# Performance work log

Hardware: AMD Instinct MI355X
Metric: run time of the kernel (lower is better)

## Reference

```python
import jax, jax.numpy as jnp
import numpy as np

N = 50000        # n_nodes
E = 640000       # n_edges
D = 128          # d_model (in_dim == out_dim)
H = 8            # num_heads
DH = D // H      # head dim = 16
EPS = 1e-5


def _batchnorm(x, g, b):
    # BatchNorm1d, training-mode batch statistics (biased variance)
    mu = jnp.mean(x, axis=0)
    var = jnp.mean((x - mu) ** 2, axis=0)
    return (x - mu) * jax.lax.rsqrt(var + EPS) * g + b


def setup_inputs() -> dict:
    key = jax.random.key(0)
    ks = jax.random.split(key, 16)
    s = 0.05
    h = jax.random.normal(ks[0], (N, D), jnp.float32)
    src = jax.random.randint(ks[1], (E,), 0, N)
    # guarantee every node has >= 1 incoming edge (avoids z == 0)
    dst = jnp.concatenate([jnp.arange(N), jax.random.randint(ks[2], (E - N,), 0, N)])
    return {
        "h": h,
        "src": src,
        "dst": dst,
        "WQ": jax.random.normal(ks[3], (D, D), jnp.float32) * s,
        "WK": jax.random.normal(ks[4], (D, D), jnp.float32) * s,
        "WV": jax.random.normal(ks[5], (D, D), jnp.float32) * s,
        "WO": jax.random.normal(ks[6], (D, D), jnp.float32) * s,
        "bO": jnp.zeros((D,), jnp.float32),
        "W1": jax.random.normal(ks[7], (2 * D, D), jnp.float32) * s,
        "b1": jnp.zeros((2 * D,), jnp.float32),
        "W2": jax.random.normal(ks[8], (D, 2 * D), jnp.float32) * s,
        "b2": jnp.zeros((D,), jnp.float32),
        "bn1_g": jnp.ones((D,), jnp.float32),
        "bn1_b": jnp.zeros((D,), jnp.float32),
        "bn2_g": jnp.ones((D,), jnp.float32),
        "bn2_b": jnp.zeros((D,), jnp.float32),
    }


def reference(h, src, dst, WQ, WK, WV, WO, bO, W1, b1, W2, b2, bn1_g, bn1_b, bn2_g, bn2_b):
    n = h.shape[0]
    # projections -> [N, H, DH]
    Q = (h @ WQ.T).reshape(n, H, DH)
    K = (h @ WK.T).reshape(n, H, DH)
    V = (h @ WV.T).reshape(n, H, DH)
    # per-edge score: sum(K[src] * Q[dst]) -> [E, H]; clamp/exp (scaled_exp)
    score = jnp.sum(K[src] * Q[dst], axis=-1) / np.sqrt(DH)
    score = jnp.exp(jnp.clip(score, -5.0, 5.0))
    # scatter-sum weighted values and normalizers to destination nodes
    wV = jax.ops.segment_sum(V[src] * score[..., None], dst, num_segments=n)  # [N,H,DH]
    z = jax.ops.segment_sum(score, dst, num_segments=n)                       # [N,H]
    attn = (wV / z[..., None]).reshape(n, D)
    # O projection + residual + BN1
    h1 = _batchnorm(h + (attn @ WO.T + bO), bn1_g, bn1_b)
    # FFN + residual + BN2
    f = jax.nn.relu(h1 @ W1.T + b1) @ W2.T + b2
    return _batchnorm(h1 + f, bn2_g, bn2_b)
```

## Files before the change

kernel.cpp:

```cpp
#include <hip/hip_runtime.h>
#include <math.h>


#define ND128 16384
typedef _Float16 f16;
typedef __attribute__((ext_vector_type(8))) _Float16 h8;
typedef __attribute__((ext_vector_type(4))) _Float16 h4;
typedef __attribute__((ext_vector_type(2))) _Float16 h2;
typedef __attribute__((ext_vector_type(4))) float f4;
typedef __attribute__((ext_vector_type(2))) float ff2;

__device__ __forceinline__ float fast_exp2(float x) {
#if __has_builtin(__builtin_amdgcn_exp2f)
    return __builtin_amdgcn_exp2f(x);
#else
    return exp2f(x);
#endif
}

template <int CTRL>
__device__ __forceinline__ float dppadd(float x) {
    int t = __builtin_amdgcn_update_dpp(0, __float_as_int(x), CTRL, 0xF, 0xF, false);
    return x + __int_as_float(t);
}
__device__ __forceinline__ float wsum8(float p) {
    p = dppadd<0xB1>(p);
    p = dppadd<0x4E>(p);
    p = dppadd<0x141>(p);
    return p;
}

__device__ __forceinline__ ff2 fp8x2_dec(unsigned v) {
#if __has_builtin(__builtin_amdgcn_cvt_pk_f32_fp8)
    return __builtin_amdgcn_cvt_pk_f32_fp8((int)v, false);
#else
    ff2 r;
    unsigned b0 = v & 0xffu, b1 = (v >> 8) & 0xffu;
    {
        unsigned e = (b0 >> 3) & 15u, m = b0 & 7u;
        float x = e ? __uint_as_float(((e + 120u) << 23) | (m << 20)) : (float)m * 0.001953125f;
        r.x = (b0 & 0x80u) ? -x : x;
    }
    {
        unsigned e = (b1 >> 3) & 15u, m = b1 & 7u;
        float x = e ? __uint_as_float(((e + 120u) << 23) | (m << 20)) : (float)m * 0.001953125f;
        r.y = (b1 & 0x80u) ? -x : x;
    }
    return r;
#endif
}

#if !__has_builtin(__builtin_amdgcn_cvt_pk_fp8_f32)
__device__ __forceinline__ unsigned char fp8_1(float f) {
    float a = fabsf(f);
    unsigned sg = (__float_as_uint(f) >> 31) << 7;
    if (a >= 448.f) return (unsigned char)(sg | 0x7E);
    if (a < 0.0009765625f) return (unsigned char)sg;
    int E; float m = frexpf(a, &E);
    if (E - 1 < -6) {
        int q = (int)rintf(a * 512.f);
        if (q > 7) return (unsigned char)(sg | 0x08);
        return (unsigned char)(sg | q);
    }
    int q = (int)rintf(m * 16.f);
    if (q == 16) { q = 8; E += 1; }
    int Ef = E - 1 + 7;
    if (Ef > 15) return (unsigned char)(sg | 0x7E);
    return (unsigned char)(sg | (Ef << 3) | (q - 8));
}
#endif

__device__ __forceinline__ unsigned fp8_pack4(float a0, float a1, float a2, float a3) {
#if __has_builtin(__builtin_amdgcn_cvt_pk_fp8_f32)
    int pk = __builtin_amdgcn_cvt_pk_fp8_f32(a0, a1, 0, false);
    pk = __builtin_amdgcn_cvt_pk_fp8_f32(a2, a3, pk, true);
    return (unsigned)pk;
#else
    return (unsigned)fp8_1(a0) | ((unsigned)fp8_1(a1) << 8) |
           ((unsigned)fp8_1(a2) << 16) | ((unsigned)fp8_1(a3) << 24);
#endif
}

__global__ __launch_bounds__(256) void k_prep_hist(
    const float* __restrict__ h, f16* __restrict__ hb,
    const float* __restrict__ WQ, const float* __restrict__ WK,
    const float* __restrict__ WV, const float* __restrict__ WO,
    const float* __restrict__ W2,
    f16* __restrict__ Wqb, f16* __restrict__ Wkb,
    f16* __restrict__ Wvb, f16* __restrict__ Wob, f16* __restrict__ W2b,
    int* __restrict__ cursor, const int* __restrict__ dst,
    int N, int E, int nhb)
{
    const int tid = threadIdx.x;
    if (blockIdx.x < (unsigned)nhb) {
        int e = blockIdx.x * 256 + tid;
        if (e < E) atomicAdd(&cursor[dst[e]], 1);
        return;
    }
    const int p = blockIdx.x - nhb;
    const int slab = p >> 1, my = p & 1;
#pragma unroll
    for (int it2 = 0; it2 < 4; ++it2) {
        int it = my * 4 + it2;
        int cid = it * 256 + tid;
        int lane = cid & 63;
        int m = (cid >> 6) & 7;
        int kb = cid >> 9;
        int row = slab * 128 + m * 16 + (lane & 15);
        int col = kb * 32 + (lane >> 4) * 8;
        f16 o8[8];
        if (row < N) {
            const float* pp = h + (size_t)row * 128 + col;
            float4 f0 = *(const float4*)pp;
            float4 f1 = *(const float4*)(pp + 4);
            o8[0] = (f16)f0.x; o8[1] = (f16)f0.y; o8[2] = (f16)f0.z; o8[3] = (f16)f0.w;
            o8[4] = (f16)f1.x; o8[5] = (f16)f1.y; o8[6] = (f16)f1.z; o8[7] = (f16)f1.w;
        } else {
#pragma unroll
            for (int j = 0; j < 8; ++j) o8[j] = (f16)0.f;
        }
        *(h8*)(hb + (size_t)slab * ND128 + (size_t)cid * 8) = *(const h8*)o8;
    }
    if (slab < 6 && my == 1) {
        const float* Wsrc; f16* dstw; int K, base;
        if (slab < 4) {
            Wsrc = slab == 0 ? WQ : slab == 1 ? WK : slab == 2 ? WV : WO;
            dstw = slab == 0 ? Wqb : slab == 1 ? Wkb : slab == 2 ? Wvb : Wob;
            K = 128; base = 0;
        } else {
            Wsrc = W2; dstw = W2b; K = 256; base = (slab - 4) * 2048;
        }
#pragma unroll
        for (int it = 0; it < 8; ++it) {
            int cid = base + it * 256 + tid;
            int lane = cid & 63;
            int kb, nt;
            if (K == 128) { kb = (cid >> 6) & 3; nt = cid >> 8; }
            else          { kb = (cid >> 6) & 7; nt = cid >> 9; }
            int row = nt * 16 + (lane & 15);
            int col = kb * 32 + (lane >> 4) * 8;
            const float* pp = Wsrc + (size_t)row * K + col;
            f16 o8[8];
#pragma unroll
            for (int j = 0; j < 8; ++j) o8[j] = (f16)pp[j];
            *(h8*)(dstw + (size_t)cid * 8) = *(const h8*)o8;
        }
    }
}

__global__ __launch_bounds__(256) void k_qkv(
    const f16* __restrict__ hb, const f16* __restrict__ Wqb,
    const f16* __restrict__ Wkb, const f16* __restrict__ Wvb,
    f16* __restrict__ Qb, unsigned char* __restrict__ KV8, int N)
{
    const int slab = blockIdx.x, oidx = blockIdx.y, mh = blockIdx.z;
    const int w = threadIdx.x >> 6, lane = threadIdx.x & 63;
    const f16* __restrict__ Wb = oidx == 0 ? Wqb : oidx == 1 ? Wkb : Wvb;
    const f16* A = hb + (size_t)slab * ND128;

    h8 bfr[2][4];
#pragma unroll
    for (int nt = 0; nt < 2; ++nt)
#pragma unroll
        for (int kb = 0; kb < 4; ++kb)
            bfr[nt][kb] = *(const h8*)(Wb + (size_t)(((2 * w + nt) * 4 + kb) * 64 + lane) * 8);

    f4 acc[4][2];
    f4 zero = {0.f, 0.f, 0.f, 0.f};
#pragma unroll
    for (int m = 0; m < 4; ++m) { acc[m][0] = zero; acc[m][1] = zero; }

#pragma unroll
    for (int m = 0; m < 4; ++m) {
        int mg = mh * 4 + m;
#pragma unroll
        for (int kb = 0; kb < 4; ++kb) {
            h8 a = *(const h8*)(A + (size_t)((kb * 8 + mg) * 64 + lane) * 8);
            acc[m][0] = __builtin_amdgcn_mfma_f32_16x16x32_f16(bfr[0][kb], a, acc[m][0], 0, 0, 0);
            acc[m][1] = __builtin_amdgcn_mfma_f32_16x16x32_f16(bfr[1][kb], a, acc[m][1], 0, 0, 0);
        }
    }

    const int rl = lane & 15, quad = lane >> 4;
    if (oidx == 0) {
#pragma unroll
        for (int m = 0; m < 4; ++m) {
            int gr = slab * 128 + (mh * 4 + m) * 16 + rl;
            if (gr < N) {
#pragma unroll
                for (int nt = 0; nt < 2; ++nt) {
                    h4 o;
                    o[0] = (f16)acc[m][nt][0]; o[1] = (f16)acc[m][nt][1];
                    o[2] = (f16)acc[m][nt][2]; o[3] = (f16)acc[m][nt][3];
                    *(h4*)(Qb + (size_t)gr * 128 + w * 32 + nt * 16 + quad * 4) = o;
                }
            }
        }
    } else {
        const int voff = (oidx == 2) ? 128 : 0;
#pragma unroll
        for (int m = 0; m < 4; ++m) {
            int gr = slab * 128 + (mh * 4 + m) * 16 + rl;
            if (gr < N) {
#pragma unroll
                for (int nt = 0; nt < 2; ++nt) {
                    unsigned pk = fp8_pack4(acc[m][nt][0], acc[m][nt][1],
                                            acc[m][nt][2], acc[m][nt][3]);
                    *(unsigned*)(KV8 + (size_t)gr * 256 + voff + w * 32 + nt * 16 + quad * 4) = pk;
                }
            }
        }
    }
}

__global__ __launch_bounds__(256) void k_scanA(
    const int* __restrict__ cnt, int* __restrict__ bsum, int N)
{
    const int t = threadIdx.x;
    int base = blockIdx.x * 2048 + t * 8;
    int s = 0;
#pragma unroll
    for (int j = 0; j < 8; ++j) {
        int idx = base + j;
        if (idx < N) s += cnt[idx];
    }
#pragma unroll
    for (int off = 32; off; off >>= 1) s += __shfl_down(s, off, 64);
    __shared__ int ws4[4];
    if ((t & 63) == 0) ws4[t >> 6] = s;
    __syncthreads();
    if (t == 0) bsum[blockIdx.x] = ws4[0] + ws4[1] + ws4[2] + ws4[3];
}

__global__ __launch_bounds__(256) void k_scanC(
    const int* __restrict__ cnt, const int* __restrict__ bsum,
    int* __restrict__ rowptr, int* __restrict__ cursor, int N, int nsb)
{
    const int t = threadIdx.x, b = blockIdx.x;
    __shared__ int sboff;
    if (t == 0) {
        int r = 0;
        for (int i2 = 0; i2 < b; ++i2) r += bsum[i2];
        sboff = r;
    }
    if (t == 64 && b == nsb - 1) {
        int r = 0;
        for (int i2 = 0; i2 < nsb; ++i2) r += bsum[i2];
        rowptr[N] = r;
    }
    int base = b * 2048 + t * 8;
    int loc[8];
    int s = 0;
#pragma unroll
    for (int j = 0; j < 8; ++j) {
        int idx = base + j;
        loc[j] = (idx < N) ? cnt[idx] : 0;
        s += loc[j];
    }
    __shared__ int part[256];
    part[t] = s;
    __syncthreads();
    for (int off = 1; off < 256; off <<= 1) {
        int v = (t >= off) ? part[t - off] : 0;
        __syncthreads();
        part[t] += v;
        __syncthreads();
    }
    int run = sboff + (t ? part[t - 1] : 0);
#pragma unroll
    for (int j = 0; j < 8; ++j) {
        int idx = base + j;
        if (idx < N) { rowptr[idx] = run; cursor[idx] = run; run += loc[j]; }
    }
}

__global__ __launch_bounds__(256) void k_scatter(
    const int* __restrict__ src, const int* __restrict__ dst,
    int* __restrict__ cursor, int* __restrict__ csr_src, int E)
{
    int e = blockIdx.x * 256 + threadIdx.x;
    if (e < E) {
        int pos = atomicAdd(&cursor[dst[e]], 1);
        csr_src[pos] = src[e];
    }
}

__global__ __launch_bounds__(256) void k_attn(
    const f16* __restrict__ Qb, const unsigned char* __restrict__ KV8,
    const int* __restrict__ rowptr, const int* __restrict__ csr_src,
    f16* __restrict__ attnf, int N)
{
    const int node = blockIdx.x * 4 + (threadIdx.x >> 6);
    const int lane = threadIdx.x & 63;
    if (node >= N) return;
    const int beg = rowptr[node], end = rowptr[node + 1];

    float qx, qy;
    {
        h2 q2 = ((const h2*)(Qb + (size_t)node * 128))[lane];
        const float SCL = 0.25f * 1.44269504f;
        qx = (float)q2[0] * SCL;
        qy = (float)q2[1] * SCL;
    }
    const float CLP = 5.f * 1.44269504f;

    float axA = 0.f, ayA = 0.f, axB = 0.f, ayB = 0.f, zA = 0.f, zB = 0.f;
    int i = beg;
    for (; i + 3 < end; i += 4) {
        int s0 = csr_src[i], s1 = csr_src[i + 1];
        int s2 = csr_src[i + 2], s3 = csr_src[i + 3];
        unsigned k0 = *(const unsigned short*)(KV8 + (size_t)s0 * 256 + 2 * lane);
        unsigned k1 = *(const unsigned short*)(KV8 + (size_t)s1 * 256 + 2 * lane);
        unsigned k2 = *(const unsigned short*)(KV8 + (size_t)s2 * 256 + 2 * lane);
        unsigned k3 = *(const unsigned short*)(KV8 + (size_t)s3 * 256 + 2 * lane);
        unsigned v0 = *(const unsigned short*)(KV8 + (size_t)s0 * 256 + 128 + 2 * lane);
        unsigned v1 = *(const unsigned short*)(KV8 + (size_t)s1 * 256 + 128 + 2 * lane);
        unsigned v2 = *(const unsigned short*)(KV8 + (size_t)s2 * 256 + 128 + 2 * lane);
        unsigned v3 = *(const unsigned short*)(KV8 + (size_t)s3 * 256 + 128 + 2 * lane);
        ff2 kf0 = fp8x2_dec(k0), kf1 = fp8x2_dec(k1);
        ff2 kf2 = fp8x2_dec(k2), kf3 = fp8x2_dec(k3);
        float p0 = fmaf(qx, kf0.x, qy * kf0.y);
        float p1 = fmaf(qx, kf1.x, qy * kf1.y);
        float p2 = fmaf(qx, kf2.x, qy * kf2.y);
        float p3 = fmaf(qx, kf3.x, qy * kf3.y);
        p0 = wsum8(p0); p1 = wsum8(p1); p2 = wsum8(p2); p3 = wsum8(p3);
        float sc0 = fast_exp2(fminf(fmaxf(p0, -CLP), CLP));
        float sc1 = fast_exp2(fminf(fmaxf(p1, -CLP), CLP));
        float sc2 = fast_exp2(fminf(fmaxf(p2, -CLP), CLP));
        float sc3 = fast_exp2(fminf(fmaxf(p3, -CLP), CLP));
        ff2 vf0 = fp8x2_dec(v0), vf1 = fp8x2_dec(v1);
        ff2 vf2 = fp8x2_dec(v2), vf3 = fp8x2_dec(v3);
        axA = fmaf(vf0.x, sc0, axA); ayA = fmaf(vf0.y, sc0, ayA);
        axB = fmaf(vf1.x, sc1, axB); ayB = fmaf(vf1.y, sc1, ayB);
        axA = fmaf(vf2.x, sc2, axA); ayA = fmaf(vf2.y, sc2, ayA);
        axB = fmaf(vf3.x, sc3, axB); ayB = fmaf(vf3.y, sc3, ayB);
        zA += sc0 + sc2; zB += sc1 + sc3;
    }
    for (; i < end; ++i) {
        int s0 = csr_src[i];
        unsigned k0 = *(const unsigned short*)(KV8 + (size_t)s0 * 256 + 2 * lane);
        unsigned v0 = *(const unsigned short*)(KV8 + (size_t)s0 * 256 + 128 + 2 * lane);
        ff2 kf0 = fp8x2_dec(k0);
        float p0 = fmaf(qx, kf0.x, qy * kf0.y);
        p0 = wsum8(p0);
        float sc0 = fast_exp2(fminf(fmaxf(p0, -CLP), CLP));
        ff2 vf0 = fp8x2_dec(v0);
        axA = fmaf(vf0.x, sc0, axA); ayA = fmaf(vf0.y, sc0, ayA);
        zA += sc0;
    }
    float inv = 1.f / (zA + zB);
    h2 o2;
    o2[0] = (f16)((axA + axB) * inv);
    o2[1] = (f16)((ayA + ayB) * inv);
    int slab = node >> 7, m = (node >> 4) & 7, lr = node & 15;
    int kb = lane >> 4, quad2 = (lane & 15) >> 2, j = (lane & 3) * 2;
    *(h2*)(attnf + (size_t)slab * ND128 +
           (size_t)(((kb * 8 + m) * 64 + lr + 16 * quad2) * 8 + j)) = o2;
}

__global__ __launch_bounds__(256) void k_oproj(
    const f16* __restrict__ attnf, const f16* __restrict__ Wob,
    const f16* __restrict__ hbf, const float* __restrict__ bO,
    f16* __restrict__ t1b, float* __restrict__ bn, int N)
{
    __shared__ float csum[128], csq[128];
    const int tid = threadIdx.x, slab = blockIdx.x, mh = blockIdx.y;
    const int w = tid >> 6, lane = tid & 63;
    if (tid < 128) { csum[tid] = 0.f; csq[tid] = 0.f; }
    __syncthreads();
    const f16* A = attnf + (size_t)slab * ND128;
    const f16* HB = hbf + (size_t)slab * ND128;

    h8 bfr[2][4];
#pragma unroll
    for (int nt = 0; nt < 2; ++nt)
#pragma unroll
        for (int kb = 0; kb < 4; ++kb)
            bfr[nt][kb] = *(const h8*)(Wob + (size_t)(((2 * w + nt) * 4 + kb) * 64 + lane) * 8);

    f4 acc[2][2];
    f4 zero = {0.f, 0.f, 0.f, 0.f};
#pragma unroll
    for (int m = 0; m < 2; ++m) { acc[m][0] = zero; acc[m][1] = zero; }
#pragma unroll
    for (int m = 0; m < 2; ++m) {
        int mg = mh * 2 + m;
#pragma unroll
        for (int kb = 0; kb < 4; ++kb) {
            h8 a = *(const h8*)(A + (size_t)((kb * 8 + mg) * 64 + lane) * 8);
            acc[m][0] = __builtin_amdgcn_mfma_f32_16x16x32_f16(bfr[0][kb], a, acc[m][0], 0, 0, 0);
            acc[m][1] = __builtin_amdgcn_mfma_f32_16x16x32_f16(bfr[1][kb], a, acc[m][1], 0, 0, 0);
        }
    }

    const int rl = lane & 15, quad = lane >> 4;
    float4 bo[2];
#pragma unroll
    for (int nt = 0; nt < 2; ++nt)
        bo[nt] = *(const float4*)(bO + w * 32 + nt * 16 + quad * 4);
    float pcs[2][4], pcq[2][4];
#pragma unroll
    for (int nt = 0; nt < 2; ++nt)
#pragma unroll
        for (int r = 0; r < 4; ++r) { pcs[nt][r] = 0.f; pcq[nt][r] = 0.f; }

#pragma unroll
    for (int m = 0; m < 2; ++m) {
        int mg = mh * 2 + m;
        int gr = slab * 128 + mg * 16 + rl;
        if (gr < N) {
#pragma unroll
            for (int nt = 0; nt < 2; ++nt) {
                size_t fidx = (size_t)(((w * 8 + mg) * 64 + (nt * 2 + (quad >> 1)) * 16 + rl) * 8 +
                                       (quad & 1) * 4);
                h4 hv4 = *(const h4*)(HB + fidx);
                float v0 = acc[m][nt][0] + (float)hv4[0] + bo[nt].x;
                float v1 = acc[m][nt][1] + (float)hv4[1] + bo[nt].y;
                float v2 = acc[m][nt][2] + (float)hv4[2] + bo[nt].z;
                float v3 = acc[m][nt][3] + (float)hv4[3] + bo[nt].w;
                h4 o; o[0] = (f16)v0; o[1] = (f16)v1; o[2] = (f16)v2; o[3] = (f16)v3;
                *(h4*)(t1b + (size_t)slab * ND128 + fidx) = o;
                pcs[nt][0] += v0; pcq[nt][0] += v0 * v0;
                pcs[nt][1] += v1; pcq[nt][1] += v1 * v1;
                pcs[nt][2] += v2; pcq[nt][2] += v2 * v2;
                pcs[nt][3] += v3; pcq[nt][3] += v3 * v3;
            }
        }
    }
#pragma unroll
    for (int nt = 0; nt < 2; ++nt)
#pragma unroll
        for (int r = 0; r < 4; ++r) {
            float s = pcs[nt][r], q = pcq[nt][r];
            s += __shfl_xor(s, 8, 16); q += __shfl_xor(q, 8, 16);
            s += __shfl_xor(s, 4, 16); q += __shfl_xor(q, 4, 16);
            s += __shfl_xor(s, 2, 16); q += __shfl_xor(q, 2, 16);
            s += __shfl_xor(s, 1, 16); q += __shfl_xor(q, 1, 16);
            if (rl == 0) {
                int cl = w * 32 + nt * 16 + quad * 4 + r;
                atomicAdd(&csum[cl], s);
                atomicAdd(&csq[cl], q);
            }
        }
    __syncthreads();
    if (tid < 128) {
        atomicAdd(bn + tid, csum[tid]);
        atomicAdd(bn + 128 + tid, csq[tid]);
    }
}

__global__ __launch_bounds__(128) void k_fold1(
    const float* __restrict__ bn, const float* __restrict__ g1,
    const float* __restrict__ bb1, const float* __restrict__ W1,
    const float* __restrict__ b1, f16* __restrict__ W1b,
    float* __restrict__ badj, float* __restrict__ sfold,
    float* __restrict__ bfold, int N)
{
    const int o = blockIdx.x, i = threadIdx.x;
    float invN = 1.f / (float)N;
    float mu = bn[i] * invN;
    float var = bn[128 + i] * invN - mu * mu;
    float s = g1[i] * rsqrtf(var + 1e-5f);
    float bb = bb1[i] - mu * s;
    if (o == 0) { sfold[i] = s; bfold[i] = bb; }
    float wv = W1[(size_t)o * 128 + i];
    __shared__ float red[128];
    red[i] = wv * bb;
    const int nt = o >> 4, lanelow = o & 15;
    const int kb = i >> 5, quad = (i >> 3) & 3, j = i & 7;
    W1b[(size_t)(((nt * 4 + kb) * 64 + lanelow + 16 * quad) * 8 + j)] = (f16)(wv * s);
    __syncthreads();
#pragma unroll
    for (int off = 64; off; off >>= 1) {
        if (i < off) red[i] += red[i + off];
        __syncthreads();
    }
    if (i == 0) badj[o] = b1[o] + red[0];
}

__global__ __launch_bounds__(256) void k_ffn1(
    const f16* __restrict__ t1b, const f16* __restrict__ W1b,
    const float* __restrict__ badj, f16* __restrict__ ub, int N)
{
    const int slab = blockIdx.x, ch = blockIdx.y, mh = blockIdx.z;
    const int w = threadIdx.x >> 6, lane = threadIdx.x & 63;
    const f16* A = t1b + (size_t)slab * ND128;

    h8 bfr[2][4];
#pragma unroll
    for (int nt = 0; nt < 2; ++nt)
#pragma unroll
        for (int kb = 0; kb < 4; ++kb) {
            int ntg = ch * 8 + 2 * w + nt;
            bfr[nt][kb] = *(const h8*)(W1b + (size_t)((ntg * 4 + kb) * 64 + lane) * 8);
        }

    f4 acc[4][2];
    f4 zero = {0.f, 0.f, 0.f, 0.f};
#pragma unroll
    for (int m = 0; m < 4; ++m) { acc[m][0] = zero; acc[m][1] = zero; }
#pragma unroll
    for (int m = 0; m < 4; ++m) {
        int mg = mh * 4 + m;
#pragma unroll
        for (int kb = 0; kb < 4; ++kb) {
            h8 a = *(const h8*)(A + (size_t)((kb * 8 + mg) * 64 + lane) * 8);
            acc[m][0] = __builtin_amdgcn_mfma_f32_16x16x32_f16(bfr[0][kb], a, acc[m][0], 0, 0, 0);
            acc[m][1] = __builtin_amdgcn_mfma_f32_16x16x32_f16(bfr[1][kb], a, acc[m][1], 0, 0, 0);
        }
    }

    const int rl = lane & 15, quad = lane >> 4;
    const int kbu = ch * 4 + w;
    float4 ba[2];
#pragma unroll
    for (int nt = 0; nt < 2; ++nt)
        ba[nt] = *(const float4*)(badj + ch * 128 + w * 32 + nt * 16 + quad * 4);
#pragma unroll
    for (int m = 0; m < 4; ++m) {
        int mg = mh * 4 + m;
        int gr = slab * 128 + mg * 16 + rl;
        if (gr < N) {
#pragma unroll
            for (int nt = 0; nt < 2; ++nt) {
                h4 o;
                o[0] = (f16)fmaxf(acc[m][nt][0] + ba[nt].x, 0.f);
                o[1] = (f16)fmaxf(acc[m][nt][1] + ba[nt].y, 0.f);
                o[2] = (f16)fmaxf(acc[m][nt][2] + ba[nt].z, 0.f);
                o[3] = (f16)fmaxf(acc[m][nt][3] + ba[nt].w, 0.f);
                *(h4*)(ub + (size_t)slab * 32768 +
                       (size_t)(((kbu * 8 + mg) * 64 + (nt * 2 + (quad >> 1)) * 16 + rl) * 8 +
                                (quad & 1) * 4)) = o;
            }
        }
    }
}

__global__ __launch_bounds__(256) void k_ffn2(
    const f16* __restrict__ ub, const f16* __restrict__ W2b,
    const f16* __restrict__ t1b,
    const float* __restrict__ sfold, const float* __restrict__ bfold,
    const float* __restrict__ b2, float* __restrict__ out,
    float* __restrict__ bn, int N)
{
    __shared__ float csum[128], csq[128], sS[128], sB[128];
    const int tid = threadIdx.x, slab = blockIdx.x, mh = blockIdx.y;
    const int w = tid >> 6, lane = tid & 63;
    if (tid < 128) {
        csum[tid] = 0.f; csq[tid] = 0.f;
        sS[tid] = sfold[tid]; sB[tid] = bfold[tid] + b2[tid];
    }
    __syncthreads();
    const f16* A = ub + (size_t)slab * 32768;
    const f16* T1 = t1b + (size_t)slab * ND128;

    h8 bfr[2][8];
#pragma unroll
    for (int nt = 0; nt < 2; ++nt)
#pragma unroll
        for (int kb = 0; kb < 8; ++kb)
            bfr[nt][kb] = *(const h8*)(W2b + (size_t)(((2 * w + nt) * 8 + kb) * 64 + lane) * 8);

    f4 acc[2][2];
    f4 zero = {0.f, 0.f, 0.f, 0.f};
#pragma unroll
    for (int m = 0; m < 2; ++m) { acc[m][0] = zero; acc[m][1] = zero; }
#pragma unroll
    for (int m = 0; m < 2; ++m) {
        int mg = mh * 2 + m;
#pragma unroll
        for (int kb = 0; kb < 8; ++kb) {
            h8 a = *(const h8*)(A + (size_t)((kb * 8 + mg) * 64 + lane) * 8);
            acc[m][0] = __builtin_amdgcn_mfma_f32_16x16x32_f16(bfr[0][kb], a, acc[m][0], 0, 0, 0);
            acc[m][1] = __builtin_amdgcn_mfma_f32_16x16x32_f16(bfr[1][kb], a, acc[m][1], 0, 0, 0);
        }
    }

    const int rl = lane & 15, quad = lane >> 4;
    float pcs[2][4], pcq[2][4];
#pragma unroll
    for (int nt = 0; nt < 2; ++nt)
#pragma unroll
        for (int r = 0; r < 4; ++r) { pcs[nt][r] = 0.f; pcq[nt][r] = 0.f; }

#pragma unroll
    for (int m = 0; m < 2; ++m) {
        int mg = mh * 2 + m;
        int gr = slab * 128 + mg * 16 + rl;
        if (gr < N) {
#pragma unroll
            for (int nt = 0; nt < 2; ++nt) {
                int col0 = w * 32 + nt * 16 + quad * 4;
                h4 t1v = *(const h4*)(T1 +
                    (size_t)(((w * 8 + mg) * 64 + (nt * 2 + (quad >> 1)) * 16 + rl) * 8 +
                             (quad & 1) * 4));
                float4 ss = *(const float4*)&sS[col0];
                float4 sb = *(const float4*)&sB[col0];
                float4 o;
                o.x = acc[m][nt][0] + fmaf(ss.x, (float)t1v[0], sb.x);
                o.y = acc[m][nt][1] + fmaf(ss.y, (float)t1v[1], sb.y);
                o.z = acc[m][nt][2] + fmaf(ss.z, (float)t1v[2], sb.z);
                o.w = acc[m][nt][3] + fmaf(ss.w, (float)t1v[3], sb.w);
                *(float4*)(out + (size_t)gr * 128 + col0) = o;
                pcs[nt][0] += o.x; pcq[nt][0] += o.x * o.x;
                pcs[nt][1] += o.y; pcq[nt][1] += o.y * o.y;
                pcs[nt][2] += o.z; pcq[nt][2] += o.z * o.z;
                pcs[nt][3] += o.w; pcq[nt][3] += o.w * o.w;
            }
        }
    }
#pragma unroll
    for (int nt = 0; nt < 2; ++nt)
#pragma unroll
        for (int r = 0; r < 4; ++r) {
            float s = pcs[nt][r], q = pcq[nt][r];
            s += __shfl_xor(s, 8, 16); q += __shfl_xor(q, 8, 16);
            s += __shfl_xor(s, 4, 16); q += __shfl_xor(q, 4, 16);
            s += __shfl_xor(s, 2, 16); q += __shfl_xor(q, 2, 16);
            s += __shfl_xor(s, 1, 16); q += __shfl_xor(q, 1, 16);
            if (rl == 0) {
                int cl = w * 32 + nt * 16 + quad * 4 + r;
                atomicAdd(&csum[cl], s);
                atomicAdd(&csq[cl], q);
            }
        }
    __syncthreads();
    if (tid < 128) {
        atomicAdd(bn + 256 + tid, csum[tid]);
        atomicAdd(bn + 384 + tid, csq[tid]);
    }
}

__global__ __launch_bounds__(256) void k_bn2(
    float* __restrict__ out, const float* __restrict__ bn,
    const float* __restrict__ g2, const float* __restrict__ bb2, int N)
{
    __shared__ float sS[128], sB[128];
    const int tid = threadIdx.x;
    if (tid < 128) {
        float invN = 1.f / (float)N;
        float mu = bn[256 + tid] * invN;
        float var = bn[384 + tid] * invN - mu * mu;
        float scl = g2[tid] * rsqrtf(var + 1e-5f);
        sS[tid] = scl;
        sB[tid] = bb2[tid] - mu * scl;
    }
    __syncthreads();
    size_t idx = (size_t)blockIdx.x * 256 + tid;
    size_t total = (size_t)N * 32;
    if (idx < total) {
        int c0 = (int)((idx * 4) & 127);
        float4 v = *(const float4*)(out + idx * 4);
        v.x = fmaf(v.x, sS[c0 + 0], sB[c0 + 0]);
        v.y = fmaf(v.y, sS[c0 + 1], sB[c0 + 1]);
        v.z = fmaf(v.z, sS[c0 + 2], sB[c0 + 2]);
        v.w = fmaf(v.w, sS[c0 + 3], sB[c0 + 3]);
        *(float4*)(out + idx * 4) = v;
    }
}

extern "C" void kernel_launch(void* const* d_in, const int* in_sizes, int n_in,
                              void* d_out, int out_size, void* d_ws, size_t ws_size,
                              hipStream_t stream)
{
    const float* h   = (const float*)d_in[0];
    const int*   src = (const int*)d_in[1];
    const int*   dst = (const int*)d_in[2];
    const float* WQ  = (const float*)d_in[3];
    const float* WK  = (const float*)d_in[4];
    const float* WV  = (const float*)d_in[5];
    const float* WO  = (const float*)d_in[6];
    const float* bO  = (const float*)d_in[7];
    const float* W1  = (const float*)d_in[8];
    const float* b1  = (const float*)d_in[9];
    const float* W2  = (const float*)d_in[10];
    const float* b2  = (const float*)d_in[11];
    const float* g1  = (const float*)d_in[12];
    const float* bb1 = (const float*)d_in[13];
    const float* g2  = (const float*)d_in[14];
    const float* bb2 = (const float*)d_in[15];
    float* out = (float*)d_out;

    int N = in_sizes[0] / 128;
    int E = in_sizes[1];
    int slabs = (N + 127) / 128;
    int nsb = (N + 2047) / 2048;
    int nhb = (E + 255) / 256;
    const size_t B1 = (size_t)slabs * 32768;

    char* Wp = (char*)d_ws;
    f16* hb  = (f16*)Wp;
    f16* Qb  = (f16*)(Wp + B1);
    unsigned char* KV8 = (unsigned char*)(Wp + 2 * B1);
    f16* attnf = (f16*)(Wp + 3 * B1);
    f16* t1b = (f16*)(Wp + 4 * B1);
    f16* ub  = (f16*)(Wp + B1);
    const size_t base = 5 * B1;
    f16* Wqb = (f16*)(Wp + base);
    f16* Wkb = (f16*)(Wp + base + 32768);
    f16* Wvb = (f16*)(Wp + base + 65536);
    f16* Wob = (f16*)(Wp + base + 98304);
    f16* W1b = (f16*)(Wp + base + 131072);
    f16* W2b = (f16*)(Wp + base + 196608);
    float* badj  = (float*)(Wp + base + 262144);
    float* sfold = (float*)(Wp + base + 263168);
    float* bfold = (float*)(Wp + base + 263680);
    float* bn    = (float*)(Wp + base + 264192);
    int* bsum    = (int*)(Wp + base + 266240);
    int* cursor  = (int*)(Wp + base + 266496);
    int* rowptr  = (int*)(Wp + base + 266496 + (size_t)N * 4);
    int* csr     = (int*)(Wp + base + 266496 + (size_t)N * 8 + 8);

    hipMemsetAsync(Wp + base + 264192, 0, 2304 + (size_t)N * 4, stream);
    k_prep_hist<<<nhb + slabs * 2, 256, 0, stream>>>(
        h, hb, WQ, WK, WV, WO, W2, Wqb, Wkb, Wvb, Wob, W2b, cursor, dst, N, E, nhb);
    k_qkv<<<dim3(slabs, 3, 2), 256, 0, stream>>>(hb, Wqb, Wkb, Wvb, Qb, KV8, N);
    k_scanA<<<nsb, 256, 0, stream>>>(cursor, bsum, N);
    k_scanC<<<nsb, 256, 0, stream>>>(cursor, bsum, rowptr, cursor, N, nsb);
    k_scatter<<<nhb, 256, 0, stream>>>(src, dst, cursor, csr, E);
    k_attn<<<(N + 3) / 4, 256, 0, stream>>>(Qb, KV8, rowptr, csr, attnf, N);
    k_oproj<<<dim3(slabs, 4), 256, 0, stream>>>(attnf, Wob, hb, bO, t1b, bn, N);
    k_fold1<<<256, 128, 0, stream>>>(bn, g1, bb1, W1, b1, W1b, badj, sfold, bfold, N);
    k_ffn1<<<dim3(slabs, 2, 2), 256, 0, stream>>>(t1b, W1b, badj, ub, N);
    k_ffn2<<<dim3(slabs, 4), 256, 0, stream>>>(ub, W2b, t1b, sfold, bfold, b2, out, bn, N);
    k_bn2<<<(int)(((size_t)N * 32 + 255) / 256), 256, 0, stream>>>(out, bn, g2, bb2, N);
}
```

Baseline: 341.6 us.

## Process full 128-row slabs per block in GEMMs; stage pre-BN2 output in fp16

Each MFMA GEMM kernel (qkv, oproj, ffn1, ffn2) now handles all 8 row groups of a slab in one block instead of splitting them across the grid, so each block loads its weight fragments once for more rows and fewer blocks are launched. The ffn2 output before BN2 is now written as fp16 in the fragment layout into the reused attention buffer, and k_bn2 reads that buffer and writes the final fp32 output. Traffic for the intermediate drops, but there are fewer blocks (less parallelism), each holding more accumulator registers, and the BN2 statistics are taken from fp16-rounded values, which adds some precision error.

```diff
diff --git a/kernel.cpp b/kernel.cpp
--- a/kernel.cpp
+++ b/kernel.cpp
@@ -153,7 +153,7 @@
     const f16* __restrict__ Wkb, const f16* __restrict__ Wvb,
     f16* __restrict__ Qb, unsigned char* __restrict__ KV8, int N)
 {
-    const int slab = blockIdx.x, oidx = blockIdx.y, mh = blockIdx.z;
+    const int slab = blockIdx.x, oidx = blockIdx.y;
     const int w = threadIdx.x >> 6, lane = threadIdx.x & 63;
     const f16* __restrict__ Wb = oidx == 0 ? Wqb : oidx == 1 ? Wkb : Wvb;
     const f16* A = hb + (size_t)slab * ND128;
@@ -165,17 +165,16 @@
         for (int kb = 0; kb < 4; ++kb)
             bfr[nt][kb] = *(const h8*)(Wb + (size_t)(((2 * w + nt) * 4 + kb) * 64 + lane) * 8);
 
-    f4 acc[4][2];
+    f4 acc[8][2];
     f4 zero = {0.f, 0.f, 0.f, 0.f};
 #pragma unroll
-    for (int m = 0; m < 4; ++m) { acc[m][0] = zero; acc[m][1] = zero; }
-
-#pragma unroll
-    for (int m = 0; m < 4; ++m) {
-        int mg = mh * 4 + m;
+    for (int m = 0; m < 8; ++m) { acc[m][0] = zero; acc[m][1] = zero; }
+
+#pragma unroll
+    for (int m = 0; m < 8; ++m) {
 #pragma unroll
         for (int kb = 0; kb < 4; ++kb) {
-            h8 a = *(const h8*)(A + (size_t)((kb * 8 + mg) * 64 + lane) * 8);
+            h8 a = *(const h8*)(A + (size_t)((kb * 8 + m) * 64 + lane) * 8);
             acc[m][0] = __builtin_amdgcn_mfma_f32_16x16x32_f16(bfr[0][kb], a, acc[m][0], 0, 0, 0);
             acc[m][1] = __builtin_amdgcn_mfma_f32_16x16x32_f16(bfr[1][kb], a, acc[m][1], 0, 0, 0);
         }
@@ -184,8 +183,8 @@
     const int rl = lane & 15, quad = lane >> 4;
     if (oidx == 0) {
 #pragma unroll
-        for (int m = 0; m < 4; ++m) {
-            int gr = slab * 128 + (mh * 4 + m) * 16 + rl;
+        for (int m = 0; m < 8; ++m) {
+            int gr = slab * 128 + m * 16 + rl;
             if (gr < N) {
 #pragma unroll
                 for (int nt = 0; nt < 2; ++nt) {
@@ -199,8 +198,8 @@
     } else {
         const int voff = (oidx == 2) ? 128 : 0;
 #pragma unroll
-        for (int m = 0; m < 4; ++m) {
-            int gr = slab * 128 + (mh * 4 + m) * 16 + rl;
+        for (int m = 0; m < 8; ++m) {
+            int gr = slab * 128 + m * 16 + rl;
             if (gr < N) {
 #pragma unroll
                 for (int nt = 0; nt < 2; ++nt) {
@@ -364,7 +363,7 @@
     f16* __restrict__ t1b, float* __restrict__ bn, int N)
 {
     __shared__ float csum[128], csq[128];
-    const int tid = threadIdx.x, slab = blockIdx.x, mh = blockIdx.y;
+    const int tid = threadIdx.x, slab = blockIdx.x;
     const int w = tid >> 6, lane = tid & 63;
     if (tid < 128) { csum[tid] = 0.f; csq[tid] = 0.f; }
     __syncthreads();
@@ -378,16 +377,15 @@
         for (int kb = 0; kb < 4; ++kb)
             bfr[nt][kb] = *(const h8*)(Wob + (size_t)(((2 * w + nt) * 4 + kb) * 64 + lane) * 8);
 
-    f4 acc[2][2];
+    f4 acc[8][2];
     f4 zero = {0.f, 0.f, 0.f, 0.f};
 #pragma unroll
-    for (int m = 0; m < 2; ++m) { acc[m][0] = zero; acc[m][1] = zero; }
-#pragma unroll
-    for (int m = 0; m < 2; ++m) {
-        int mg = mh * 2 + m;
+    for (int m = 0; m < 8; ++m) { acc[m][0] = zero; acc[m][1] = zero; }
+#pragma unroll
+    for (int m = 0; m < 8; ++m) {
 #pragma unroll
         for (int kb = 0; kb < 4; ++kb) {
-            h8 a = *(const h8*)(A + (size_t)((kb * 8 + mg) * 64 + lane) * 8);
+            h8 a = *(const h8*)(A + (size_t)((kb * 8 + m) * 64 + lane) * 8);
             acc[m][0] = __builtin_amdgcn_mfma_f32_16x16x32_f16(bfr[0][kb], a, acc[m][0], 0, 0, 0);
             acc[m][1] = __builtin_amdgcn_mfma_f32_16x16x32_f16(bfr[1][kb], a, acc[m][1], 0, 0, 0);
         }
@@ -405,13 +403,12 @@
         for (int r = 0; r < 4; ++r) { pcs[nt][r] = 0.f; pcq[nt][r] = 0.f; }
 
 #pragma unroll
-    for (int m = 0; m < 2; ++m) {
-        int mg = mh * 2 + m;
-        int gr = slab * 128 + mg * 16 + rl;
+    for (int m = 0; m < 8; ++m) {
+        int gr = slab * 128 + m * 16 + rl;
         if (gr < N) {
 #pragma unroll
             for (int nt = 0; nt < 2; ++nt) {
-                size_t fidx = (size_t)(((w * 8 + mg) * 64 + (nt * 2 + (quad >> 1)) * 16 + rl) * 8 +
+                size_t fidx = (size_t)(((w * 8 + m) * 64 + (nt * 2 + (quad >> 1)) * 16 + rl) * 8 +
                                        (quad & 1) * 4);
                 h4 hv4 = *(const h4*)(HB + fidx);
                 float v0 = acc[m][nt][0] + (float)hv4[0] + bo[nt].x;
@@ -482,7 +479,7 @@
     const f16* __restrict__ t1b, const f16* __restrict__ W1b,
     const float* __restrict__ badj, f16* __restrict__ ub, int N)
 {
-    const int slab = blockIdx.x, ch = blockIdx.y, mh = blockIdx.z;
+    const int slab = blockIdx.x, ch = blockIdx.y;
     const int w = threadIdx.x >> 6, lane = threadIdx.x & 63;
     const f16* A = t1b + (size_t)slab * ND128;
 
@@ -495,16 +492,15 @@
             bfr[nt][kb] = *(const h8*)(W1b + (size_t)((ntg * 4 + kb) * 64 + lane) * 8);
         }
 
-    f4 acc[4][2];
+    f4 acc[8][2];
     f4 zero = {0.f, 0.f, 0.f, 0.f};
 #pragma unroll
-    for (int m = 0; m < 4; ++m) { acc[m][0] = zero; acc[m][1] = zero; }
-#pragma unroll
-    for (int m = 0; m < 4; ++m) {
-        int mg = mh * 4 + m;
+    for (int m = 0; m < 8; ++m) { acc[m][0] = zero; acc[m][1] = zero; }
+#pragma unroll
+    for (int m = 0; m < 8; ++m) {
 #pragma unroll
         for (int kb = 0; kb < 4; ++kb) {
-            h8 a = *(const h8*)(A + (size_t)((kb * 8 + mg) * 64 + lane) * 8);
+            h8 a = *(const h8*)(A + (size_t)((kb * 8 + m) * 64 + lane) * 8);
             acc[m][0] = __builtin_amdgcn_mfma_f32_16x16x32_f16(bfr[0][kb], a, acc[m][0], 0, 0, 0);
             acc[m][1] = __builtin_amdgcn_mfma_f32_16x16x32_f16(bfr[1][kb], a, acc[m][1], 0, 0, 0);
         }
@@ -517,9 +513,8 @@
     for (int nt = 0; nt < 2; ++nt)
         ba[nt] = *(const float4*)(badj + ch * 128 + w * 32 + nt * 16 + quad * 4);
 #pragma unroll
-    for (int m = 0; m < 4; ++m) {
-        int mg = mh * 4 + m;
-        int gr = slab * 128 + mg * 16 + rl;
+    for (int m = 0; m < 8; ++m) {
+        int gr = slab * 128 + m * 16 + rl;
         if (gr < N) {
 #pragma unroll
             for (int nt = 0; nt < 2; ++nt) {
@@ -529,7 +524,7 @@
                 o[2] = (f16)fmaxf(acc[m][nt][2] + ba[nt].z, 0.f);
                 o[3] = (f16)fmaxf(acc[m][nt][3] + ba[nt].w, 0.f);
                 *(h4*)(ub + (size_t)slab * 32768 +
-                       (size_t)(((kbu * 8 + mg) * 64 + (nt * 2 + (quad >> 1)) * 16 + rl) * 8 +
+                       (size_t)(((kbu * 8 + m) * 64 + (nt * 2 + (quad >> 1)) * 16 + rl) * 8 +
                                 (quad & 1) * 4)) = o;
             }
         }
@@ -540,11 +535,11 @@
     const f16* __restrict__ ub, const f16* __restrict__ W2b,
     const f16* __restrict__ t1b,
     const float* __restrict__ sfold, const float* __restrict__ bfold,
-    const float* __restrict__ b2, float* __restrict__ out,
+    const float* __restrict__ b2, f16* __restrict__ t2f,
     float* __restrict__ bn, int N)
 {
     __shared__ float csum[128], csq[128], sS[128], sB[128];
-    const int tid = threadIdx.x, slab = blockIdx.x, mh = blockIdx.y;
+    const int tid = threadIdx.x, slab = blockIdx.x;
     const int w = tid >> 6, lane = tid & 63;
     if (tid < 128) {
         csum[tid] = 0.f; csq[tid] = 0.f;
@@ -561,16 +556,15 @@
         for (int kb = 0; kb < 8; ++kb)
             bfr[nt][kb] = *(const h8*)(W2b + (size_t)(((2 * w + nt) * 8 + kb) * 64 + lane) * 8);
 
-    f4 acc[2][2];
+    f4 acc[8][2];
     f4 zero = {0.f, 0.f, 0.f, 0.f};
 #pragma unroll
-    for (int m = 0; m < 2; ++m) { acc[m][0] = zero; acc[m][1] = zero; }
-#pragma unroll
-    for (int m = 0; m < 2; ++m) {
-        int mg = mh * 2 + m;
+    for (int m = 0; m < 8; ++m) { acc[m][0] = zero; acc[m][1] = zero; }
+#pragma unroll
+    for (int m = 0; m < 8; ++m) {
 #pragma unroll
         for (int kb = 0; kb < 8; ++kb) {
-            h8 a = *(const h8*)(A + (size_t)((kb * 8 + mg) * 64 + lane) * 8);
+            h8 a = *(const h8*)(A + (size_t)((kb * 8 + m) * 64 + lane) * 8);
             acc[m][0] = __builtin_amdgcn_mfma_f32_16x16x32_f16(bfr[0][kb], a, acc[m][0], 0, 0, 0);
             acc[m][1] = __builtin_amdgcn_mfma_f32_16x16x32_f16(bfr[1][kb], a, acc[m][1], 0, 0, 0);
         }
@@ -584,28 +578,29 @@
         for (int r = 0; r < 4; ++r) { pcs[nt][r] = 0.f; pcq[nt][r] = 0.f; }
 
 #pragma unroll
-    for (int m = 0; m < 2; ++m) {
-        int mg = mh * 2 + m;
-        int gr = slab * 128 + mg * 16 + rl;
+    for (int m = 0; m < 8; ++m) {
+        int gr = slab * 128 + m * 16 + rl;
         if (gr < N) {
 #pragma unroll
             for (int nt = 0; nt < 2; ++nt) {
                 int col0 = w * 32 + nt * 16 + quad * 4;
-                h4 t1v = *(const h4*)(T1 +
-                    (size_t)(((w * 8 + mg) * 64 + (nt * 2 + (quad >> 1)) * 16 + rl) * 8 +
-                             (quad & 1) * 4));
+                size_t fidx = (size_t)(((w * 8 + m) * 64 + (nt * 2 + (quad >> 1)) * 16 + rl) * 8 +
+                                       (quad & 1) * 4);
+                h4 t1v = *(const h4*)(T1 + fidx);
                 float4 ss = *(const float4*)&sS[col0];
                 float4 sb = *(const float4*)&sB[col0];
-                float4 o;
-                o.x = acc[m][nt][0] + fmaf(ss.x, (float)t1v[0], sb.x);
-                o.y = acc[m][nt][1] + fmaf(ss.y, (float)t1v[1], sb.y);
-                o.z = acc[m][nt][2] + fmaf(ss.z, (float)t1v[2], sb.z);
-                o.w = acc[m][nt][3] + fmaf(ss.w, (float)t1v[3], sb.w);
-                *(float4*)(out + (size_t)gr * 128 + col0) = o;
-                pcs[nt][0] += o.x; pcq[nt][0] += o.x * o.x;
-                pcs[nt][1] += o.y; pcq[nt][1] += o.y * o.y;
-                pcs[nt][2] += o.z; pcq[nt][2] += o.z * o.z;
-                pcs[nt][3] += o.w; pcq[nt][3] += o.w * o.w;
+                h4 o2;
+                o2[0] = (f16)(acc[m][nt][0] + fmaf(ss.x, (float)t1v[0], sb.x));
+                o2[1] = (f16)(acc[m][nt][1] + fmaf(ss.y, (float)t1v[1], sb.y));
+                o2[2] = (f16)(acc[m][nt][2] + fmaf(ss.z, (float)t1v[2], sb.z));
+                o2[3] = (f16)(acc[m][nt][3] + fmaf(ss.w, (float)t1v[3], sb.w));
+                *(h4*)(t2f + (size_t)slab * ND128 + fidx) = o2;
+                float r0 = (float)o2[0], r1 = (float)o2[1];
+                float r2 = (float)o2[2], r3 = (float)o2[3];
+                pcs[nt][0] += r0; pcq[nt][0] += r0 * r0;
+                pcs[nt][1] += r1; pcq[nt][1] += r1 * r1;
+                pcs[nt][2] += r2; pcq[nt][2] += r2 * r2;
+                pcs[nt][3] += r3; pcq[nt][3] += r3 * r3;
             }
         }
     }
@@ -632,7 +627,8 @@
 }
 
 __global__ __launch_bounds__(256) void k_bn2(
-    float* __restrict__ out, const float* __restrict__ bn,
+    const f16* __restrict__ t2f, float* __restrict__ out,
+    const float* __restrict__ bn,
     const float* __restrict__ g2, const float* __restrict__ bb2, int N)
 {
     __shared__ float sS[128], sB[128];
@@ -649,13 +645,19 @@
     size_t idx = (size_t)blockIdx.x * 256 + tid;
     size_t total = (size_t)N * 32;
     if (idx < total) {
-        int c0 = (int)((idx * 4) & 127);
-        float4 v = *(const float4*)(out + idx * 4);
-        v.x = fmaf(v.x, sS[c0 + 0], sB[c0 + 0]);
-        v.y = fmaf(v.y, sS[c0 + 1], sB[c0 + 1]);
-        v.z = fmaf(v.z, sS[c0 + 2], sB[c0 + 2]);
-        v.w = fmaf(v.w, sS[c0 + 3], sB[c0 + 3]);
-        *(float4*)(out + idx * 4) = v;
+        int gr = (int)(idx >> 5);
+        int c0 = ((int)idx & 31) * 4;
+        int slab = gr >> 7, m = (gr >> 4) & 7, rl = gr & 15;
+        int w = c0 >> 5, nt = (c0 >> 4) & 1, q = (c0 >> 2) & 3;
+        size_t fidx = (size_t)(((w * 8 + m) * 64 + (nt * 2 + (q >> 1)) * 16 + rl) * 8 +
+                               (q & 1) * 4);
+        h4 v = *(const h4*)(t2f + (size_t)slab * ND128 + fidx);
+        float4 o;
+        o.x = fmaf((float)v[0], sS[c0 + 0], sB[c0 + 0]);
+        o.y = fmaf((float)v[1], sS[c0 + 1], sB[c0 + 1]);
+        o.z = fmaf((float)v[2], sS[c0 + 2], sB[c0 + 2]);
+        o.w = fmaf((float)v[3], sS[c0 + 3], sB[c0 + 3]);
+        *(float4*)(out + (size_t)gr * 128 + c0) = o;
     }
 }
 
@@ -695,6 +697,7 @@
     f16* attnf = (f16*)(Wp + 3 * B1);
     f16* t1b = (f16*)(Wp + 4 * B1);
     f16* ub  = (f16*)(Wp + B1);
+    f16* t2f = attnf;
     const size_t base = 5 * B1;
     f16* Wqb = (f16*)(Wp + base);
     f16* Wkb = (f16*)(Wp + base + 32768);
@@ -714,14 +717,14 @@
     hipMemsetAsync(Wp + base + 264192, 0, 2304 + (size_t)N * 4, stream);
     k_prep_hist<<<nhb + slabs * 2, 256, 0, stream>>>(
         h, hb, WQ, WK, WV, WO, W2, Wqb, Wkb, Wvb, Wob, W2b, cursor, dst, N, E, nhb);
-    k_qkv<<<dim3(slabs, 3, 2), 256, 0, stream>>>(hb, Wqb, Wkb, Wvb, Qb, KV8, N);
+    k_qkv<<<dim3(slabs, 3), 256, 0, stream>>>(hb, Wqb, Wkb, Wvb, Qb, KV8, N);
     k_scanA<<<nsb, 256, 0, stream>>>(cursor, bsum, N);
     k_scanC<<<nsb, 256, 0, stream>>>(cursor, bsum, rowptr, cursor, N, nsb);
     k_scatter<<<nhb, 256, 0, stream>>>(src, dst, cursor, csr, E);
     k_attn<<<(N + 3) / 4, 256, 0, stream>>>(Qb, KV8, rowptr, csr, attnf, N);
-    k_oproj<<<dim3(slabs, 4), 256, 0, stream>>>(attnf, Wob, hb, bO, t1b, bn, N);
+    k_oproj<<<slabs, 256, 0, stream>>>(attnf, Wob, hb, bO, t1b, bn, N);
     k_fold1<<<256, 128, 0, stream>>>(bn, g1, bb1, W1, b1, W1b, badj, sfold, bfold, N);
-    k_ffn1<<<dim3(slabs, 2, 2), 256, 0, stream>>>(t1b, W1b, badj, ub, N);
-    k_ffn2<<<dim3(slabs, 4), 256, 0, stream>>>(ub, W2b, t1b, sfold, bfold, b2, out, bn, N);
-    k_bn2<<<(int)(((size_t)N * 32 + 255) / 256), 256, 0, stream>>>(out, bn, g2, bb2, N);
-}
+    k_ffn1<<<dim3(slabs, 2), 256, 0, stream>>>(t1b, W1b, badj, ub, N);
+    k_ffn2<<<slabs, 256, 0, stream>>>(ub, W2b, t1b, sfold, bfold, b2, t2f, bn, N);
+    k_bn2<<<(int)(((size_t)N * 32 + 255) / 256), 256, 0, stream>>>(t2f, out, bn, g2, bb2, N);
+}
```

Measured after the change: 308.4 us. -9.7%, faster.
